# Kernel optimization log

Hardware: AMD Instinct MI355X
Metric: run time of the kernel (lower is better)

The kernel has to match this reference:

```python
import jax, jax.numpy as jnp
import numpy as np

B, S, D, H = 4, 2048, 1024, 16
DEPTH = D // H
NEG = -1000000000.0


def setup_inputs() -> dict:
    key = jax.random.key(0)
    ks = jax.random.split(key, 11)
    scale = 1.0 / np.sqrt(D)
    return {
        "q": jax.random.normal(ks[0], (B, S, D), jnp.float32),
        "k": jax.random.normal(ks[1], (B, S, D), jnp.float32),
        "v": jax.random.normal(ks[2], (B, S, D), jnp.float32),
        "wq_w": jax.random.normal(ks[3], (D, D), jnp.float32) * scale,
        "wq_b": jax.random.normal(ks[4], (D,), jnp.float32) * 0.01,
        "wk_w": jax.random.normal(ks[5], (D, D), jnp.float32) * scale,
        "wk_b": jax.random.normal(ks[6], (D,), jnp.float32) * 0.01,
        "wv_w": jax.random.normal(ks[7], (D, D), jnp.float32) * scale,
        "wv_b": jax.random.normal(ks[8], (D,), jnp.float32) * 0.01,
        "dense_w": jax.random.normal(ks[9], (D, D), jnp.float32) * scale,
        "dense_b": jax.random.normal(ks[10], (D,), jnp.float32) * 0.01,
    }


def _split_heads(x):
    # (B, S, D) -> (B, H, S, depth)
    b, s, _ = x.shape
    return x.reshape(b, s, H, DEPTH).transpose(0, 2, 1, 3)


def reference(q, k, v, wq_w, wq_b, wk_w, wk_b, wv_w, wv_b, dense_w, dense_b):
    b, s, _ = q.shape
    qh = _split_heads(q @ wq_w.T + wq_b)
    kh = _split_heads(k @ wk_w.T + wk_b)
    vh = _split_heads(v @ wv_w.T + wv_b)
    logits = jnp.einsum('bhqd,bhkd->bhqk', qh, kh) / np.sqrt(DEPTH).astype(np.float32)
    # additive causal mask (strict upper triangle = -1e9)
    mask = jnp.where(jnp.triu(jnp.ones((s, s), jnp.float32), k=1) == 1.0, NEG, 0.0)
    logits = logits + mask
    attn = jax.nn.softmax(logits, axis=-1)
    out = jnp.einsum('bhqk,bhkd->bhqd', attn, vh)
    out = out.transpose(0, 2, 1, 3).reshape(b, s, D)
    return out @ dense_w.T + dense_b
```

## Files before the change

kernel.cpp:

```cpp
#include <hip/hip_runtime.h>
#include <hip/hip_bf16.h>


typedef __attribute__((ext_vector_type(8))) short bf16x8;
typedef __attribute__((ext_vector_type(4))) float f32x4;
typedef __attribute__((ext_vector_type(8))) unsigned short u16x8;

#define MFMA16(a, b, c) __builtin_amdgcn_mfma_f32_16x16x32_bf16(a, b, c, 0, 0, 0)

#define GLOAD_LDS16(gp, lp)                                                    \
  __builtin_amdgcn_global_load_lds(                                            \
      (const __attribute__((address_space(1))) void*)(gp),                     \
      (__attribute__((address_space(3))) void*)(lp), 16, 0, 0)

__device__ __forceinline__ unsigned short f2bf(float f) {
  union { float f; unsigned u; } x; x.f = f;
  unsigned u = x.u;
  return (unsigned short)((u + 0x7fffu + ((u >> 16) & 1u)) >> 16);
}

__device__ __forceinline__ unsigned pk2(float a, float b) {
  union { __hip_bfloat162 h; unsigned u; } cv;
  cv.h = __float22bfloat162_rn(float2{a, b});
  return cv.u;
}

__global__ __launch_bounds__(256) void convert_kernel(
    const float* __restrict__ q, const float* __restrict__ k,
    const float* __restrict__ v, const float* __restrict__ wq,
    const float* __restrict__ wk, const float* __restrict__ wv,
    const float* __restrict__ wd, const float* __restrict__ bq,
    const float* __restrict__ bk, const float* __restrict__ bv,
    unsigned short* __restrict__ dst, float* __restrict__ bias_pack) {
  const size_t tid0 = (size_t)blockIdx.x * blockDim.x + threadIdx.x;
  const size_t nthreads = (size_t)gridDim.x * blockDim.x;
  if (tid0 < 3072) {
    bias_pack[tid0] = tid0 < 1024 ? bq[tid0]
                     : (tid0 < 2048 ? bk[tid0 - 1024] : bv[tid0 - 2048]);
  }
  const size_t NQ = 8192ull * 1024;
  const size_t NW = 1024ull * 1024;
  const size_t total_chunks = (3 * NQ + 4 * NW) / 8;
  for (size_t c = tid0; c < total_chunks; c += nthreads) {
    const size_t e = c * 8;
    const float* src;
    if (e < NQ) src = q + e;
    else if (e < 2 * NQ) src = k + (e - NQ);
    else if (e < 3 * NQ) src = v + (e - 2 * NQ);
    else {
      const size_t we = e - 3 * NQ;
      if (we < NW) src = wq + we;
      else if (we < 2 * NW) src = wk + (we - NW);
      else if (we < 3 * NW) src = wv + (we - 2 * NW);
      else src = wd + (we - 3 * NW);
    }
    f32x4 a = *(const f32x4*)(src);
    f32x4 b = *(const f32x4*)(src + 4);
    u16x8 o;
    o[0] = f2bf(a[0]); o[1] = f2bf(a[1]); o[2] = f2bf(a[2]); o[3] = f2bf(a[3]);
    o[4] = f2bf(b[0]); o[5] = f2bf(b[1]); o[6] = f2bf(b[2]); o[7] = f2bf(b[3]);
    *(u16x8*)(dst + e) = o;
  }
}

template <int MODE>
__global__ __launch_bounds__(256) void gemm_kernel(
    const unsigned short* __restrict__ Abase,
    const unsigned short* __restrict__ Wbase,
    const float* __restrict__ biasbase, unsigned short* __restrict__ dstb,
    float* __restrict__ dstf) {
  __shared__ __attribute__((aligned(16))) unsigned short Ablk[128 * 32];
  __shared__ __attribute__((aligned(16))) unsigned short Bblk[128 * 32];
  const size_t NQ = 8192ull * 1024, NW = 1024ull * 1024;
  int flat = ((int)blockIdx.z * 64 + blockIdx.y) * 8 + blockIdx.x;
  const int cpx = (gridDim.x * gridDim.y * gridDim.z) >> 3;
  flat = (flat & 7) * cpx + (flat >> 3);
  const int bz = flat >> 9;
  const int rem = flat & 511;
  const int by = rem >> 3, bx = rem & 7;

  const int z = bz;
  const unsigned short* A;
  const unsigned short* W;
  int m0, n0;
  if (MODE == 0 && z == 2) {
    A = Wbase + 2 * NW;
    W = Abase + 2 * NQ;
    m0 = bx * 128;
    n0 = by * 128;
  } else {
    A = Abase + (size_t)z * NQ;
    W = Wbase + (size_t)z * NW;
    m0 = by * 128;
    n0 = bx * 128;
  }
  const float* bias = biasbase + (size_t)z * 1024;
  const int tid = threadIdx.x, lane = tid & 63, w = tid >> 6;
  const int wr = (w >> 1) * 64, wc = (w & 1) * 64;
  const int llo = lane & 15, lhi = lane >> 4;
  f32x4 acc[4][4] = {};
  const unsigned short* ag = A + (size_t)(m0 + (tid >> 2)) * 1024 + (tid & 3) * 8;
  const unsigned short* wg = W + (size_t)(n0 + (tid >> 2)) * 1024 + (tid & 3) * 8;
  unsigned short* lA = &Ablk[tid * 8];
  unsigned short* lA2 = &Ablk[2048 + tid * 8];
  unsigned short* lB = &Bblk[tid * 8];
  unsigned short* lB2 = &Bblk[2048 + tid * 8];
  for (int kt = 0; kt < 32; ++kt) {
    const int ko = kt * 32;
    if (kt) __syncthreads();
    GLOAD_LDS16(ag + ko, lA);
    GLOAD_LDS16(ag + ko + 64 * 1024, lA2);
    GLOAD_LDS16(wg + ko, lB);
    GLOAD_LDS16(wg + ko + 64 * 1024, lB2);
    __syncthreads();
    bf16x8 af[4], bfr[4];
#pragma unroll
    for (int i = 0; i < 4; ++i)
      af[i] = *(const bf16x8*)&Ablk[(wr + i * 16 + llo) * 32 + lhi * 8];
#pragma unroll
    for (int i = 0; i < 4; ++i)
      bfr[i] = *(const bf16x8*)&Bblk[(wc + i * 16 + llo) * 32 + lhi * 8];
#pragma unroll
    for (int mi = 0; mi < 4; ++mi)
#pragma unroll
      for (int ni = 0; ni < 4; ++ni)
        acc[mi][ni] = MFMA16(af[mi], bfr[ni], acc[mi][ni]);
  }
  const float osc = (MODE == 0 && z == 0) ? 0.1803368801f : 1.0f;
#pragma unroll
  for (int mi = 0; mi < 4; ++mi) {
#pragma unroll
    for (int ni = 0; ni < 4; ++ni) {
      const int n = n0 + wc + ni * 16 + llo;
      const float bv = (MODE == 0) ? ((z == 2) ? 0.f : bias[n]) : bias[n];
#pragma unroll
      for (int r = 0; r < 4; ++r) {
        const int m = m0 + wr + mi * 16 + lhi * 4 + r;
        float val = acc[mi][ni][r] + bv;
        if (MODE == 1) {
          dstf[(size_t)m * 1024 + n] = val;
        } else if (z < 2) {
          val *= osc;
          const int b = m >> 11, s = m & 2047, h = n >> 6, d = n & 63;
          dstb[(size_t)z * NQ +
               (((size_t)(b * 16 + h) * 2048 + s) * 64 + d)] = f2bf(val);
        } else {
          val = acc[mi][ni][r] + bias[m];
          const int h = m >> 6, d = m & 63, b = n >> 11, sidx = n & 2047;
          const int t = sidx & 63;
          const int ps = (sidx & ~63) | ((t & 15) << 2) | (t >> 4);
          dstb[2 * NQ + (((size_t)(b * 16 + h) * 64 + d) * 2048 + ps)] = f2bf(val);
        }
      }
    }
  }
}

__global__ __launch_bounds__(256, 2) void attn_kernel(
    const unsigned short* __restrict__ Qp, const unsigned short* __restrict__ Kp,
    const unsigned short* __restrict__ Vtp, unsigned short* __restrict__ attn_out) {
  __shared__ __attribute__((aligned(16))) unsigned short Klds[2][64 * 64];
  __shared__ __attribute__((aligned(16))) unsigned short Vt[2][64 * 64];
  __shared__ __attribute__((aligned(16))) unsigned short Plds[4 * 32 * 72];
  const int flat = (int)blockIdx.x;
  const int xcd = flat & 7, idx = flat >> 3;
  const int bh = xcd * 8 + (idx >> 3);
  const int pr = idx & 7;
  const int tid = threadIdx.x, lane = tid & 63, w = tid >> 6;
  const int llo = lane & 15, lhi = lane >> 4;
  const int qbase[2] = {pr * 128 + w * 32, (15 - pr) * 128 + w * 32};

  bf16x8 qf[2][2][2];
#pragma unroll
  for (int t = 0; t < 2; ++t)
#pragma unroll
    for (int mi = 0; mi < 2; ++mi) {
      const unsigned short* qptr =
          Qp + ((size_t)bh * 2048 + qbase[t] + mi * 16 + llo) * 64 + lhi * 8;
      qf[t][mi][0] = *(const bf16x8*)qptr;
      qf[t][mi][1] = *(const bf16x8*)(qptr + 32);
    }

  bf16x8 ones;
#pragma unroll
  for (int i = 0; i < 8; ++i) ones[i] = (short)0x3F80;

  f32x4 o[2][2][5] = {};

  const size_t kbase = (size_t)bh * (64 * 2048);
  const int r0 = tid >> 3, r1 = r0 + 32;
  const int scb = (tid & 7) * 16;
  const int kcol0 = (scb ^ ((r0 & 7) << 4)) >> 1;
  const int kcol1 = (scb ^ ((r1 & 7) << 4)) >> 1;
  const int koff0 = r0 * 64 + kcol0, koff1 = r1 * 64 + kcol1;
  const int voff0 = r0 * 2048 + kcol0, voff1 = r1 * 2048 + kcol1;
  unsigned short* pw = &Plds[w * (32 * 72)];

  const int nkt = 2 * (16 - pr);

#define STAGE(buf, kv0_)                                                       \
  do {                                                                         \
    GLOAD_LDS16(Kp + kbase + (size_t)(kv0_)*64 + koff0, &Klds[buf][tid * 8]);  \
    GLOAD_LDS16(Kp + kbase + (size_t)(kv0_)*64 + koff1,                        \
                &Klds[buf][2048 + tid * 8]);                                   \
    GLOAD_LDS16(Vtp + kbase + (kv0_) + voff0, &Vt[buf][tid * 8]);              \
    GLOAD_LDS16(Vtp + kbase + (kv0_) + voff1, &Vt[buf][2048 + tid * 8]);       \
  } while (0)

  STAGE(0, 0);
  __syncthreads();

  for (int kt = 0; kt < nkt; ++kt) {
    const int kv0 = kt * 64;
    const int cb = kt & 1;
    if (kt + 1 < nkt) STAGE(cb ^ 1, kv0 + 64);

#pragma unroll
    for (int t = 0; t < 2; ++t) {
      const int qb = qbase[t];
      if (kv0 <= qb + 31) {
        f32x4 s[2][4] = {};
        __builtin_amdgcn_s_setprio(1);
#pragma unroll
        for (int b4 = 0; b4 < 4; ++b4) {
          const int row = b4 * 16 + llo;
          const int sw = (row & 7) << 3;
          const bf16x8 k0 =
              *(const bf16x8*)&Klds[cb][row * 64 + ((lhi * 8) ^ sw)];
          const bf16x8 k1 =
              *(const bf16x8*)&Klds[cb][row * 64 + ((32 + lhi * 8) ^ sw)];
          s[0][b4] = MFMA16(qf[t][0][0], k0, s[0][b4]);
          s[0][b4] = MFMA16(qf[t][0][1], k1, s[0][b4]);
          s[1][b4] = MFMA16(qf[t][1][0], k0, s[1][b4]);
          s[1][b4] = MFMA16(qf[t][1][1], k1, s[1][b4]);
        }
        __builtin_amdgcn_s_setprio(0);

        const bool needm = (kv0 + 63 > qb);
#pragma unroll
        for (int mi = 0; mi < 2; ++mi) {
#pragma unroll
          for (int r = 0; r < 4; ++r) {
            float sv0 = s[mi][0][r], sv1 = s[mi][1][r];
            float sv2 = s[mi][2][r], sv3 = s[mi][3][r];
            if (needm) {
              const int qrow = qb + mi * 16 + lhi * 4 + r;
              if (kv0 + llo > qrow) sv0 = -1e9f;
              if (kv0 + 16 + llo > qrow) sv1 = -1e9f;
              if (kv0 + 32 + llo > qrow) sv2 = -1e9f;
              if (kv0 + 48 + llo > qrow) sv3 = -1e9f;
            }
            const float p0 = exp2f(sv0), p1 = exp2f(sv1);
            const float p2 = exp2f(sv2), p3 = exp2f(sv3);
            const int prow = mi * 16 + lhi * 4 + r;
            *(uint2*)&pw[prow * 72 + llo * 4] =
                make_uint2(pk2(p0, p1), pk2(p2, p3));
          }
        }

        bf16x8 pa[2][2];
#pragma unroll
        for (int mi = 0; mi < 2; ++mi) {
          pa[mi][0] = *(const bf16x8*)&pw[(mi * 16 + llo) * 72 + lhi * 8];
          pa[mi][1] = *(const bf16x8*)&pw[(mi * 16 + llo) * 72 + 32 + lhi * 8];
        }
        __builtin_amdgcn_s_setprio(1);
#pragma unroll
        for (int dblk = 0; dblk < 4; ++dblk) {
          const int row = dblk * 16 + llo;
          const int sw = (row & 7) << 3;
          const bf16x8 v0 =
              *(const bf16x8*)&Vt[cb][row * 64 + ((lhi * 8) ^ sw)];
          const bf16x8 v1 =
              *(const bf16x8*)&Vt[cb][row * 64 + ((32 + lhi * 8) ^ sw)];
          o[t][0][dblk] = MFMA16(pa[0][0], v0, o[t][0][dblk]);
          o[t][0][dblk] = MFMA16(pa[0][1], v1, o[t][0][dblk]);
          o[t][1][dblk] = MFMA16(pa[1][0], v0, o[t][1][dblk]);
          o[t][1][dblk] = MFMA16(pa[1][1], v1, o[t][1][dblk]);
        }
        o[t][0][4] = MFMA16(pa[0][0], ones, o[t][0][4]);
        o[t][0][4] = MFMA16(pa[0][1], ones, o[t][0][4]);
        o[t][1][4] = MFMA16(pa[1][0], ones, o[t][1][4]);
        o[t][1][4] = MFMA16(pa[1][1], ones, o[t][1][4]);
        __builtin_amdgcn_s_setprio(0);
      }
    }

    __syncthreads();
  }
#undef STAGE

  const int b = bh >> 4, h = bh & 15;
#pragma unroll
  for (int t = 0; t < 2; ++t) {
#pragma unroll
    for (int mi = 0; mi < 2; ++mi) {
#pragma unroll
      for (int r = 0; r < 4; ++r) {
        const float inv = 1.0f / o[t][mi][4][r];
        const int qrow = qbase[t] + mi * 16 + lhi * 4 + r;
        const size_t base = ((size_t)b * 2048 + qrow) * 1024 + h * 64;
#pragma unroll
        for (int dblk = 0; dblk < 4; ++dblk)
          attn_out[base + dblk * 16 + llo] = f2bf(o[t][mi][dblk][r] * inv);
      }
    }
  }
}

extern "C" void kernel_launch(void* const* d_in, const int* in_sizes, int n_in,
                              void* d_out, int out_size, void* d_ws,
                              size_t ws_size, hipStream_t stream) {
  const float* q = (const float*)d_in[0];
  const float* k = (const float*)d_in[1];
  const float* v = (const float*)d_in[2];
  const float* wq_w = (const float*)d_in[3];
  const float* wq_b = (const float*)d_in[4];
  const float* wk_w = (const float*)d_in[5];
  const float* wk_b = (const float*)d_in[6];
  const float* wv_w = (const float*)d_in[7];
  const float* wv_b = (const float*)d_in[8];
  const float* dense_w = (const float*)d_in[9];
  const float* dense_b = (const float*)d_in[10];
  float* out = (float*)d_out;

  char* ws = (char*)d_ws;
  const size_t MB = 1024ull * 1024;
  unsigned short* qkv_bf = (unsigned short*)(ws);
  unsigned short* w_bf = (unsigned short*)(ws + 48 * MB);
  float* bias_pack = (float*)(ws + 56 * MB);
  unsigned short* qkvp = (unsigned short*)(ws + 57 * MB);
  unsigned short* attn_o = (unsigned short*)(ws + 105 * MB);
  const size_t PEL = 8192ull * 1024;

  convert_kernel<<<dim3(2048), dim3(256), 0, stream>>>(
      q, k, v, wq_w, wk_w, wv_w, dense_w, wq_b, wk_b, wv_b, qkv_bf, bias_pack);

  gemm_kernel<0><<<dim3(8, 64, 3), dim3(256), 0, stream>>>(
      qkv_bf, w_bf, bias_pack, qkvp, nullptr);

  attn_kernel<<<dim3(512), dim3(256), 0, stream>>>(
      qkvp, qkvp + PEL, qkvp + 2 * PEL, attn_o);

  gemm_kernel<1><<<dim3(8, 64, 1), dim3(256), 0, stream>>>(
      attn_o, w_bf + 3ull * 1024 * 1024, dense_b, nullptr, out);
}
```

Baseline: 210.1 us.

## Rewrite projection GEMMs as 8-wave triple-buffered kernel with swizzled LDS

Replaces the single-buffered 128x128 GEMM with a 512-thread, 128x256 tile kernel that uses K-tiles of 64, triple-buffered LDS staging through direct global-to-LDS loads, and explicit vmcnt waits, so copies overlap the MFMA work. LDS rows get an XOR swizzle to cut bank conflicts. The QKV projection is split into two launches (Q/K, and a transposed V mode), and setprio brackets the MFMA sections. The cost is more LDS per block (about 144KB), which limits occupancy, and hand-tuned waitcnt logic that is fragile.

```diff
diff --git a/kernel.cpp b/kernel.cpp
--- a/kernel.cpp
+++ b/kernel.cpp
@@ -64,92 +64,145 @@
 }
 
 template <int MODE>
-__global__ __launch_bounds__(256) void gemm_kernel(
+__global__ __launch_bounds__(512, 2) void gemm8_kernel(
     const unsigned short* __restrict__ Abase,
     const unsigned short* __restrict__ Wbase,
     const float* __restrict__ biasbase, unsigned short* __restrict__ dstb,
     float* __restrict__ dstf) {
-  __shared__ __attribute__((aligned(16))) unsigned short Ablk[128 * 32];
-  __shared__ __attribute__((aligned(16))) unsigned short Bblk[128 * 32];
+  __shared__ __attribute__((aligned(16))) unsigned short Ablk[3][128 * 64];
+  __shared__ __attribute__((aligned(16))) unsigned short Bblk[3][256 * 64];
   const size_t NQ = 8192ull * 1024, NW = 1024ull * 1024;
-  int flat = ((int)blockIdx.z * 64 + blockIdx.y) * 8 + blockIdx.x;
-  const int cpx = (gridDim.x * gridDim.y * gridDim.z) >> 3;
-  flat = (flat & 7) * cpx + (flat >> 3);
-  const int bz = flat >> 9;
-  const int rem = flat & 511;
-  const int by = rem >> 3, bx = rem & 7;
-
-  const int z = bz;
+  const int nx = gridDim.x, ny = gridDim.y;
+  const int tot = nx * ny * (int)gridDim.z;
+  int flat = ((int)blockIdx.z * ny + blockIdx.y) * nx + blockIdx.x;
+  flat = (flat & 7) * (tot >> 3) + (flat >> 3);
+  const int bx = flat % nx;
+  const int tmp = flat / nx;
+  const int by = tmp % ny;
+  const int z = tmp / ny;
+
   const unsigned short* A;
   const unsigned short* W;
-  int m0, n0;
-  if (MODE == 0 && z == 2) {
-    A = Wbase + 2 * NW;
-    W = Abase + 2 * NQ;
-    m0 = bx * 128;
-    n0 = by * 128;
-  } else {
-    A = Abase + (size_t)z * NQ;
-    W = Wbase + (size_t)z * NW;
-    m0 = by * 128;
-    n0 = bx * 128;
-  }
-  const float* bias = biasbase + (size_t)z * 1024;
+  if (MODE == 0) { A = Abase + (size_t)z * NQ; W = Wbase + (size_t)z * NW; }
+  else if (MODE == 2) { A = Wbase + 2 * NW; W = Abase + 2 * NQ; }
+  else { A = Abase; W = Wbase; }
+  const int m0 = by * 128, n0 = bx * 256;
+
   const int tid = threadIdx.x, lane = tid & 63, w = tid >> 6;
-  const int wr = (w >> 1) * 64, wc = (w & 1) * 64;
+  const int wm = w >> 2, wn = w & 3;
   const int llo = lane & 15, lhi = lane >> 4;
+
+  int srcA[2], srcB[4];
+#pragma unroll
+  for (int j = 0; j < 4; ++j) {
+    const int c = tid + j * 512;
+    const int off = (c >> 3) * 1024 + ((((c & 7) ^ ((c >> 3) & 7))) << 3);
+    if (j < 2) srcA[j] = off;
+    srcB[j] = off;
+  }
+  const unsigned short* Ag = A + (size_t)m0 * 1024;
+  const unsigned short* Wg = W + (size_t)n0 * 1024;
+
+#define STA(bi, kt_, j)                                                        \
+  GLOAD_LDS16(Ag + srcA[j] + (kt_) * 64,                                       \
+              (unsigned short*)Ablk[bi] + (tid + (j) * 512) * 8)
+#define STB(bi, kt_, j)                                                        \
+  GLOAD_LDS16(Wg + srcB[j] + (kt_) * 64,                                       \
+              (unsigned short*)Bblk[bi] + (tid + (j) * 512) * 8)
+
   f32x4 acc[4][4] = {};
-  const unsigned short* ag = A + (size_t)(m0 + (tid >> 2)) * 1024 + (tid & 3) * 8;
-  const unsigned short* wg = W + (size_t)(n0 + (tid >> 2)) * 1024 + (tid & 3) * 8;
-  unsigned short* lA = &Ablk[tid * 8];
-  unsigned short* lA2 = &Ablk[2048 + tid * 8];
-  unsigned short* lB = &Bblk[tid * 8];
-  unsigned short* lB2 = &Bblk[2048 + tid * 8];
-  for (int kt = 0; kt < 32; ++kt) {
-    const int ko = kt * 32;
-    if (kt) __syncthreads();
-    GLOAD_LDS16(ag + ko, lA);
-    GLOAD_LDS16(ag + ko + 64 * 1024, lA2);
-    GLOAD_LDS16(wg + ko, lB);
-    GLOAD_LDS16(wg + ko + 64 * 1024, lB2);
-    __syncthreads();
-    bf16x8 af[4], bfr[4];
-#pragma unroll
-    for (int i = 0; i < 4; ++i)
-      af[i] = *(const bf16x8*)&Ablk[(wr + i * 16 + llo) * 32 + lhi * 8];
-#pragma unroll
-    for (int i = 0; i < 4; ++i)
-      bfr[i] = *(const bf16x8*)&Bblk[(wc + i * 16 + llo) * 32 + lhi * 8];
+  const int cswz0 = ((lhi ^ (llo & 7)) << 3);
+  const int cswz1 = (((4 + lhi) ^ (llo & 7)) << 3);
+
+  STA(0, 0, 0); STA(0, 0, 1);
+  STB(0, 0, 0); STB(0, 0, 1); STB(0, 0, 2); STB(0, 0, 3);
+  STA(1, 1, 0); STA(1, 1, 1);
+  STB(1, 1, 0); STB(1, 1, 1); STB(1, 1, 2); STB(1, 1, 3);
+
+#pragma unroll
+  for (int kt = 0; kt < 16; ++kt) {
+    const int cb = kt % 3, nb = (kt + 2) % 3;
+    __builtin_amdgcn_s_barrier();
+    __builtin_amdgcn_sched_barrier(0);
+    if (kt + 2 < 16) { STA(nb, kt + 2, 0); STA(nb, kt + 2, 1); STB(nb, kt + 2, 0); }
+    if (kt <= 13) asm volatile("s_waitcnt vmcnt(9)" ::: "memory");
+    else if (kt == 14) asm volatile("s_waitcnt vmcnt(6)" ::: "memory");
+    else asm volatile("s_waitcnt vmcnt(0)" ::: "memory");
+    __builtin_amdgcn_s_barrier();
+    __builtin_amdgcn_sched_barrier(0);
+
+    bf16x8 af[4][2], bf01[2][2];
+#pragma unroll
+    for (int mi = 0; mi < 4; ++mi) {
+      const int ar = (wm * 64 + mi * 16 + llo) * 64;
+      af[mi][0] = *(const bf16x8*)&Ablk[cb][ar + cswz0];
+      af[mi][1] = *(const bf16x8*)&Ablk[cb][ar + cswz1];
+    }
+#pragma unroll
+    for (int ni = 0; ni < 2; ++ni) {
+      const int br = (wn * 64 + ni * 16 + llo) * 64;
+      bf01[ni][0] = *(const bf16x8*)&Bblk[cb][br + cswz0];
+      bf01[ni][1] = *(const bf16x8*)&Bblk[cb][br + cswz1];
+    }
+    __builtin_amdgcn_s_setprio(1);
 #pragma unroll
     for (int mi = 0; mi < 4; ++mi)
 #pragma unroll
-      for (int ni = 0; ni < 4; ++ni)
-        acc[mi][ni] = MFMA16(af[mi], bfr[ni], acc[mi][ni]);
-  }
+      for (int ni = 0; ni < 2; ++ni) {
+        acc[mi][ni] = MFMA16(af[mi][0], bf01[ni][0], acc[mi][ni]);
+        acc[mi][ni] = MFMA16(af[mi][1], bf01[ni][1], acc[mi][ni]);
+      }
+    __builtin_amdgcn_s_setprio(0);
+    __builtin_amdgcn_s_barrier();
+    __builtin_amdgcn_sched_barrier(0);
+
+    if (kt + 2 < 16) { STB(nb, kt + 2, 1); STB(nb, kt + 2, 2); STB(nb, kt + 2, 3); }
+    bf16x8 bf23[2][2];
+#pragma unroll
+    for (int ni = 0; ni < 2; ++ni) {
+      const int br = (wn * 64 + (ni + 2) * 16 + llo) * 64;
+      bf23[ni][0] = *(const bf16x8*)&Bblk[cb][br + cswz0];
+      bf23[ni][1] = *(const bf16x8*)&Bblk[cb][br + cswz1];
+    }
+    __builtin_amdgcn_s_setprio(1);
+#pragma unroll
+    for (int mi = 0; mi < 4; ++mi)
+#pragma unroll
+      for (int ni = 0; ni < 2; ++ni) {
+        acc[mi][ni + 2] = MFMA16(af[mi][0], bf23[ni][0], acc[mi][ni + 2]);
+        acc[mi][ni + 2] = MFMA16(af[mi][1], bf23[ni][1], acc[mi][ni + 2]);
+      }
+    __builtin_amdgcn_s_setprio(0);
+  }
+#undef STA
+#undef STB
+
   const float osc = (MODE == 0 && z == 0) ? 0.1803368801f : 1.0f;
+  const float* bias = (MODE == 0) ? biasbase + (size_t)z * 1024
+                     : (MODE == 2) ? biasbase + 2048 : biasbase;
 #pragma unroll
   for (int mi = 0; mi < 4; ++mi) {
 #pragma unroll
     for (int ni = 0; ni < 4; ++ni) {
-      const int n = n0 + wc + ni * 16 + llo;
-      const float bv = (MODE == 0) ? ((z == 2) ? 0.f : bias[n]) : bias[n];
+      const int n = n0 + wn * 64 + ni * 16 + llo;
+      const int mbase = m0 + wm * 64 + mi * 16 + lhi * 4;
 #pragma unroll
       for (int r = 0; r < 4; ++r) {
-        const int m = m0 + wr + mi * 16 + lhi * 4 + r;
-        float val = acc[mi][ni][r] + bv;
+        const int m = mbase + r;
         if (MODE == 1) {
-          dstf[(size_t)m * 1024 + n] = val;
-        } else if (z < 2) {
-          val *= osc;
+          dstf[(size_t)m * 1024 + n] = acc[mi][ni][r] + bias[n];
+        } else if (MODE == 0) {
+          const float val = (acc[mi][ni][r] + bias[n]) * osc;
           const int b = m >> 11, s = m & 2047, h = n >> 6, d = n & 63;
-          dstb[(size_t)z * NQ +
-               (((size_t)(b * 16 + h) * 2048 + s) * 64 + d)] = f2bf(val);
+          dstb[(size_t)z * NQ + (((size_t)(b * 16 + h) * 2048 + s) * 64 + d)] =
+              f2bf(val);
         } else {
-          val = acc[mi][ni][r] + bias[m];
+          const float val = acc[mi][ni][r] + bias[m];
           const int h = m >> 6, d = m & 63, b = n >> 11, sidx = n & 2047;
           const int t = sidx & 63;
           const int ps = (sidx & ~63) | ((t & 15) << 2) | (t >> 4);
-          dstb[2 * NQ + (((size_t)(b * 16 + h) * 64 + d) * 2048 + ps)] = f2bf(val);
+          dstb[2 * NQ + (((size_t)(b * 16 + h) * 64 + d) * 2048 + ps)] =
+              f2bf(val);
         }
       }
     }
@@ -336,12 +389,15 @@
   convert_kernel<<<dim3(2048), dim3(256), 0, stream>>>(
       q, k, v, wq_w, wk_w, wv_w, dense_w, wq_b, wk_b, wv_b, qkv_bf, bias_pack);
 
-  gemm_kernel<0><<<dim3(8, 64, 3), dim3(256), 0, stream>>>(
+  gemm8_kernel<0><<<dim3(4, 64, 2), dim3(512), 0, stream>>>(
+      qkv_bf, w_bf, bias_pack, qkvp, nullptr);
+
+  gemm8_kernel<2><<<dim3(32, 8, 1), dim3(512), 0, stream>>>(
       qkv_bf, w_bf, bias_pack, qkvp, nullptr);
 
   attn_kernel<<<dim3(512), dim3(256), 0, stream>>>(
       qkvp, qkvp + PEL, qkvp + 2 * PEL, attn_o);
 
-  gemm_kernel<1><<<dim3(8, 64, 1), dim3(256), 0, stream>>>(
+  gemm8_kernel<1><<<dim3(4, 64, 1), dim3(512), 0, stream>>>(
       attn_o, w_bf + 3ull * 1024 * 1024, dense_b, nullptr, out);
 }
```

Result: faster. 200.0 us (-4.8%).
